# Optimization experiments

Measured on AMD Instinct MI355X. Metric: run time of the kernel, lower is better.

The kernel has to match this reference:

```python
import jax, jax.numpy as jnp
import numpy as np

MARGIN = 0.2
EPS = 1e-6  # torch.pairwise_distance adds eps to the difference before the norm


def setup_inputs() -> dict:
    key = jax.random.key(0)
    k1, k2, k3 = jax.random.split(key, 3)
    B, D = 8192, 128
    emb1 = jax.random.normal(k1, (B, D), dtype=jnp.float32)
    emb2 = jax.random.normal(k2, (B, D), dtype=jnp.float32)
    target = jax.random.randint(k3, (B,), 0, 2, dtype=jnp.int64)
    return {"emb1": emb1, "emb2": emb2, "target": target}


def reference(emb1, emb2, target):
    B, D = emb1.shape
    # torch.pairwise_distance(a, b) = ||a - b + EPS||_2; expand the square:
    # |a-b+eps|^2 = |a|^2 + |b|^2 - 2 a.b + 2*eps*(sum(a)-sum(b)) + D*eps^2
    sq = (
        jnp.sum(emb1 * emb1, axis=-1)[:, None]
        + jnp.sum(emb2 * emb2, axis=-1)[None, :]
        - 2.0 * (emb1 @ emb2.T)
        + 2.0 * EPS * (jnp.sum(emb1, axis=-1)[:, None] - jnp.sum(emb2, axis=-1)[None, :])
        + D * EPS * EPS
    )
    dist = jnp.sqrt(jnp.maximum(sq, 0.0))  # [B, B]: dist[i, j] = ||emb1[i] - emb2[j] + eps||

    pos = target == 1
    neg = target == 0
    # hardest positive: max over columns j with target[j]==1; hardest negative: min over target[j]==0
    pos_max = jnp.max(jnp.where(pos[None, :], dist, -jnp.inf), axis=1)  # [B]
    neg_min = jnp.min(jnp.where(neg[None, :], dist, jnp.inf), axis=1)   # [B]
    per_anchor = jnp.maximum(pos_max - neg_min + MARGIN, 0.0)
    anchor_w = pos.astype(dist.dtype)
    # mean over anchors (rows i with target[i]==1)
    return jnp.sum(per_anchor * anchor_w) / jnp.sum(anchor_w)
```

## Files before the change

kernel.cpp:

```cpp
#include <hip/hip_runtime.h>
#include <hip/hip_bf16.h>
#include <math.h>


#define DDIM   128
#define SPLITS 8
#define MARGIN 0.2f
#define EPS    1e-6f
#define SENT   1e30f

typedef unsigned short ushort_t;
typedef __attribute__((ext_vector_type(8))) short short8;
typedef __attribute__((ext_vector_type(8))) unsigned short ushort8;
typedef __attribute__((ext_vector_type(4))) float f32x4;

__device__ __forceinline__ ushort_t f2bf(float f) {
    unsigned int u = __float_as_uint(f);
    u = (u + 0x7FFFu + ((u >> 16) & 1u)) >> 16;
    return (ushort_t)u;
}

__global__ void prep_kernel(const float* __restrict__ e1, const float* __restrict__ e2,
                            const int* __restrict__ target,
                            float* __restrict__ rowterm,
                            float* __restrict__ cpos, float* __restrict__ cneg, int B) {
    int w    = (blockIdx.x * blockDim.x + threadIdx.x) >> 6;
    int lane = threadIdx.x & 63;
    if (w >= 2 * B) return;
    bool first = (w < B);
    int r = first ? w : w - B;
    const float* src = (first ? e1 : e2) + (size_t)r * DDIM;
    float2 v = *(const float2*)(src + lane * 2);
    float s = v.x + v.y;
    float n = v.x * v.x + v.y * v.y;
    #pragma unroll
    for (int off = 32; off > 0; off >>= 1) {
        s += __shfl_down(s, off, 64);
        n += __shfl_down(n, off, 64);
    }
    if (lane == 0) {
        if (first) {
            rowterm[r] = n + 2.f * EPS * s + (float)DDIM * EPS * EPS;
        } else {
            float ct = n - 2.f * EPS * s;
            int tg = target[r];
            cpos[r] = (tg == 1) ? ct : -SENT;
            cneg[r] = (tg == 0) ? ct :  SENT;
        }
    }
}

__device__ __forceinline__ void stage_tile(const float* __restrict__ g,
                                           ushort_t* __restrict__ lds, int tid) {
    #pragma unroll
    for (int it = 0; it < 8; ++it) {
        int idx = it * 256 + tid;
        int r   = idx >> 4;
        int c8  = idx & 15;
        const float* src = g + (size_t)r * DDIM + c8 * 8;
        float4 v0 = *(const float4*)src;
        float4 v1 = *(const float4*)(src + 4);
        ushort8 o;
        o[0] = f2bf(v0.x); o[1] = f2bf(v0.y); o[2] = f2bf(v0.z); o[3] = f2bf(v0.w);
        o[4] = f2bf(v1.x); o[5] = f2bf(v1.y); o[6] = f2bf(v1.z); o[7] = f2bf(v1.w);
        int pos = c8 ^ (r & 15);
        *(ushort8*)(lds + r * DDIM + pos * 8) = o;
    }
}

__global__ __launch_bounds__(256, 2)
void tile_kernel(const float* __restrict__ e1, const float* __restrict__ e2,
                 const float* __restrict__ cpos, const float* __restrict__ cneg,
                 float* __restrict__ pmp, float* __restrict__ nmp, int B) {
    __shared__ __align__(16) ushort_t As[128 * DDIM];
    __shared__ __align__(16) ushort_t Bs[128 * DDIM];

    const int tid = threadIdx.x;
    const int w   = tid >> 6;
    const int l   = tid & 63;
    const int lq  = l >> 4;
    const int lm  = l & 15;
    const int row0 = blockIdx.x * 128;
    const int colSpan = B / SPLITS;
    const int col0 = blockIdx.y * colSpan;
    const int nTiles = colSpan / 128;

    stage_tile(e1 + (size_t)row0 * DDIM, As, tid);

    const int wr = (w >> 1) * 64;
    const int wc = (w & 1) * 64;

    float pm[4][4], nm[4][4];
    #pragma unroll
    for (int i = 0; i < 4; ++i)
        #pragma unroll
        for (int r = 0; r < 4; ++r) { pm[i][r] = -SENT; nm[i][r] = SENT; }

    const ushort_t* aRow = As + (wr + lm) * DDIM;
    const ushort_t* bRow = Bs + (wc + lm) * DDIM;

    for (int t = 0; t < nTiles; ++t) {
        if (t) __syncthreads();
        stage_tile(e2 + (size_t)(col0 + t * 128) * DDIM, Bs, tid);
        __syncthreads();

        f32x4 acc[4][4];
        #pragma unroll
        for (int i = 0; i < 4; ++i)
            #pragma unroll
            for (int j = 0; j < 4; ++j)
                acc[i][j] = (f32x4){0.f, 0.f, 0.f, 0.f};

        #pragma unroll
        for (int kk = 0; kk < DDIM; kk += 32) {
            const int co = (((lq + (kk >> 3)) ^ lm) << 3);
            short8 af[4], bf[4];
            #pragma unroll
            for (int i = 0; i < 4; ++i)
                af[i] = *(const short8*)(aRow + i * 16 * DDIM + co);
            #pragma unroll
            for (int j = 0; j < 4; ++j)
                bf[j] = *(const short8*)(bRow + j * 16 * DDIM + co);
            #pragma unroll
            for (int i = 0; i < 4; ++i)
                #pragma unroll
                for (int j = 0; j < 4; ++j)
                    acc[i][j] = __builtin_amdgcn_mfma_f32_16x16x32_bf16(
                                    af[i], bf[j], acc[i][j], 0, 0, 0);
        }

        #pragma unroll
        for (int j = 0; j < 4; ++j) {
            int col = col0 + t * 128 + wc + j * 16 + lm;
            float cp = cpos[col];
            float cn = cneg[col];
            #pragma unroll
            for (int i = 0; i < 4; ++i)
                #pragma unroll
                for (int r = 0; r < 4; ++r) {
                    float d = acc[i][j][r];
                    pm[i][r] = fmaxf(pm[i][r], fmaf(-2.f, d, cp));
                    nm[i][r] = fminf(nm[i][r], fmaf(-2.f, d, cn));
                }
        }
    }

    #pragma unroll
    for (int m = 1; m < 16; m <<= 1) {
        #pragma unroll
        for (int i = 0; i < 4; ++i)
            #pragma unroll
            for (int r = 0; r < 4; ++r) {
                pm[i][r] = fmaxf(pm[i][r], __shfl_xor(pm[i][r], m, 64));
                nm[i][r] = fminf(nm[i][r], __shfl_xor(nm[i][r], m, 64));
            }
    }

    __syncthreads();
    float* smP = (float*)As;
    float* smN = smP + 128;
    if ((w & 1) == 1 && lm == 0) {
        #pragma unroll
        for (int i = 0; i < 4; ++i)
            #pragma unroll
            for (int r = 0; r < 4; ++r) {
                int lr = wr + i * 16 + lq * 4 + r;
                smP[lr] = pm[i][r];
                smN[lr] = nm[i][r];
            }
    }
    __syncthreads();
    if ((w & 1) == 0 && lm == 0) {
        #pragma unroll
        for (int i = 0; i < 4; ++i)
            #pragma unroll
            for (int r = 0; r < 4; ++r) {
                int lr  = wr + i * 16 + lq * 4 + r;
                int row = row0 + lr;
                pmp[(size_t)blockIdx.y * B + row] = fmaxf(pm[i][r], smP[lr]);
                nmp[(size_t)blockIdx.y * B + row] = fminf(nm[i][r], smN[lr]);
            }
    }
}

__global__ void reduce_kernel(const float* __restrict__ pmp, const float* __restrict__ nmp,
                              const float* __restrict__ rowterm, const int* __restrict__ target,
                              float* __restrict__ out, int B) {
    float s = 0.f, c = 0.f;
    for (int row = threadIdx.x; row < B; row += blockDim.x) {
        float pmv = -SENT, nmv = SENT;
        #pragma unroll
        for (int sp = 0; sp < SPLITS; ++sp) {
            pmv = fmaxf(pmv, pmp[(size_t)sp * B + row]);
            nmv = fminf(nmv, nmp[(size_t)sp * B + row]);
        }
        float rt = rowterm[row];
        float dp = sqrtf(fmaxf(rt + pmv, 0.f));
        float dn = sqrtf(fmaxf(rt + nmv, 0.f));
        if (target[row] == 1) {
            s += fmaxf(dp - dn + MARGIN, 0.f);
            c += 1.f;
        }
    }
    #pragma unroll
    for (int off = 32; off > 0; off >>= 1) {
        s += __shfl_down(s, off, 64);
        c += __shfl_down(c, off, 64);
    }
    __shared__ float ls[16], lc[16];
    int wv = threadIdx.x >> 6, ln = threadIdx.x & 63;
    if (ln == 0) { ls[wv] = s; lc[wv] = c; }
    __syncthreads();
    if (threadIdx.x == 0) {
        float ss = 0.f, cc = 0.f;
        int nw = blockDim.x >> 6;
        for (int i = 0; i < nw; ++i) { ss += ls[i]; cc += lc[i]; }
        out[0] = ss / cc;
    }
}

extern "C" void kernel_launch(void* const* d_in, const int* in_sizes, int n_in,
                              void* d_out, int out_size, void* d_ws, size_t ws_size,
                              hipStream_t stream) {
    const float* e1     = (const float*)d_in[0];
    const float* e2     = (const float*)d_in[1];
    const int*   target = (const int*)d_in[2];
    float* out = (float*)d_out;
    const int B = in_sizes[2];

    float* p = (float*)d_ws;
    float* rowterm = p;              p += B;
    float* cpos    = p;              p += B;
    float* cneg    = p;              p += B;
    float* pmp     = p;              p += (size_t)SPLITS * B;
    float* nmp     = p;

    {
        int blocks = (2 * B + 3) / 4;
        prep_kernel<<<blocks, 256, 0, stream>>>(e1, e2, target, rowterm, cpos, cneg, B);
    }
    {
        dim3 grid(B / 128, SPLITS);
        tile_kernel<<<grid, 256, 0, stream>>>(e1, e2, cpos, cneg, pmp, nmp, B);
    }
    reduce_kernel<<<1, 1024, 0, stream>>>(pmp, nmp, rowterm, target, out, B);
}
```

Before: 99.32 us.

## Pre-convert embeddings to bf16 and stage tiles via direct global-to-LDS loads

The prep kernel now writes bf16 copies of both embedding matrices, so the tile kernel no longer reloads fp32 data and converts it on every column tile. The tile kernel then stages tiles with global_load_lds DMA into a padded chunk layout, which removes the VGPR round trip and drops the XOR swizzle. The final reduction is spread over 32 blocks that combine through atomics and a ticket counter instead of running as a single block. This adds an extra bf16 write pass and workspace in prep, and relies on the padded pitch to avoid LDS bank conflicts.

```diff
diff --git a/kernel.cpp b/kernel.cpp
--- a/kernel.cpp
+++ b/kernel.cpp
@@ -9,9 +9,12 @@
 #define EPS    1e-6f
 #define SENT   1e30f
 
+#define CHUNK_PITCH 1056
+#define WAVE_SPAN   (8 * CHUNK_PITCH)
+#define TILE_BYTES  (4 * WAVE_SPAN)
+
 typedef unsigned short ushort_t;
 typedef __attribute__((ext_vector_type(8))) short short8;
-typedef __attribute__((ext_vector_type(8))) unsigned short ushort8;
 typedef __attribute__((ext_vector_type(4))) float f32x4;
 
 __device__ __forceinline__ ushort_t f2bf(float f) {
@@ -20,10 +23,22 @@
     return (ushort_t)u;
 }
 
+__device__ __forceinline__ void g2lds16(const ushort_t* g, void* lds) {
+    __builtin_amdgcn_global_load_lds(
+        (const __attribute__((address_space(1))) unsigned int*)g,
+        (__attribute__((address_space(3))) unsigned int*)lds,
+        16, 0, 0);
+}
+
 __global__ void prep_kernel(const float* __restrict__ e1, const float* __restrict__ e2,
                             const int* __restrict__ target,
+                            ushort_t* __restrict__ e1b, ushort_t* __restrict__ e2b,
                             float* __restrict__ rowterm,
-                            float* __restrict__ cpos, float* __restrict__ cneg, int B) {
+                            float* __restrict__ cpos, float* __restrict__ cneg,
+                            float* __restrict__ redsum, int* __restrict__ ticket, int B) {
+    if (blockIdx.x == 0 && threadIdx.x == 0) {
+        redsum[0] = 0.f; redsum[1] = 0.f; *ticket = 0;
+    }
     int w    = (blockIdx.x * blockDim.x + threadIdx.x) >> 6;
     int lane = threadIdx.x & 63;
     if (w >= 2 * B) return;
@@ -31,6 +46,9 @@
     int r = first ? w : w - B;
     const float* src = (first ? e1 : e2) + (size_t)r * DDIM;
     float2 v = *(const float2*)(src + lane * 2);
+    ushort_t* dst = (first ? e1b : e2b) + (size_t)r * DDIM;
+    ushort2 o; o.x = f2bf(v.x); o.y = f2bf(v.y);
+    *(ushort2*)(dst + lane * 2) = o;
     float s = v.x + v.y;
     float n = v.x * v.x + v.y * v.y;
     #pragma unroll
@@ -50,30 +68,22 @@
     }
 }
 
-__device__ __forceinline__ void stage_tile(const float* __restrict__ g,
-                                           ushort_t* __restrict__ lds, int tid) {
-    #pragma unroll
-    for (int it = 0; it < 8; ++it) {
-        int idx = it * 256 + tid;
-        int r   = idx >> 4;
-        int c8  = idx & 15;
-        const float* src = g + (size_t)r * DDIM + c8 * 8;
-        float4 v0 = *(const float4*)src;
-        float4 v1 = *(const float4*)(src + 4);
-        ushort8 o;
-        o[0] = f2bf(v0.x); o[1] = f2bf(v0.y); o[2] = f2bf(v0.z); o[3] = f2bf(v0.w);
-        o[4] = f2bf(v1.x); o[5] = f2bf(v1.y); o[6] = f2bf(v1.z); o[7] = f2bf(v1.w);
-        int pos = c8 ^ (r & 15);
-        *(ushort8*)(lds + r * DDIM + pos * 8) = o;
-    }
+__device__ __forceinline__ void stage_tile_dma(const ushort_t* __restrict__ gRow0,
+                                               unsigned char* __restrict__ lds,
+                                               int w, int l) {
+    const ushort_t* g = gRow0 + (size_t)(w * 32) * DDIM + l * 8;
+    unsigned char* lp = lds + w * WAVE_SPAN;
+    #pragma unroll
+    for (int it = 0; it < 8; ++it)
+        g2lds16(g + it * 512, lp + it * CHUNK_PITCH);
 }
 
 __global__ __launch_bounds__(256, 2)
-void tile_kernel(const float* __restrict__ e1, const float* __restrict__ e2,
+void tile_kernel(const ushort_t* __restrict__ e1b, const ushort_t* __restrict__ e2b,
                  const float* __restrict__ cpos, const float* __restrict__ cneg,
                  float* __restrict__ pmp, float* __restrict__ nmp, int B) {
-    __shared__ __align__(16) ushort_t As[128 * DDIM];
-    __shared__ __align__(16) ushort_t Bs[128 * DDIM];
+    __shared__ __align__(16) unsigned char As[TILE_BYTES];
+    __shared__ __align__(16) unsigned char Bs[TILE_BYTES];
 
     const int tid = threadIdx.x;
     const int w   = tid >> 6;
@@ -85,7 +95,7 @@
     const int col0 = blockIdx.y * colSpan;
     const int nTiles = colSpan / 128;
 
-    stage_tile(e1 + (size_t)row0 * DDIM, As, tid);
+    stage_tile_dma(e1b + (size_t)row0 * DDIM, As, w, l);
 
     const int wr = (w >> 1) * 64;
     const int wc = (w & 1) * 64;
@@ -96,12 +106,14 @@
         #pragma unroll
         for (int r = 0; r < 4; ++r) { pm[i][r] = -SENT; nm[i][r] = SENT; }
 
-    const ushort_t* aRow = As + (wr + lm) * DDIM;
-    const ushort_t* bRow = Bs + (wc + lm) * DDIM;
+    const unsigned char* aLane = As + ((wr >> 2) + (lm >> 2)) * CHUNK_PITCH
+                                    + (lm & 3) * 256 + lq * 16;
+    const unsigned char* bLane = Bs + ((wc >> 2) + (lm >> 2)) * CHUNK_PITCH
+                                    + (lm & 3) * 256 + lq * 16;
 
     for (int t = 0; t < nTiles; ++t) {
         if (t) __syncthreads();
-        stage_tile(e2 + (size_t)(col0 + t * 128) * DDIM, Bs, tid);
+        stage_tile_dma(e2b + (size_t)(col0 + t * 128) * DDIM, Bs, w, l);
         __syncthreads();
 
         f32x4 acc[4][4];
@@ -113,14 +125,14 @@
 
         #pragma unroll
         for (int kk = 0; kk < DDIM; kk += 32) {
-            const int co = (((lq + (kk >> 3)) ^ lm) << 3);
+            const int ko = kk * 2;
             short8 af[4], bf[4];
             #pragma unroll
             for (int i = 0; i < 4; ++i)
-                af[i] = *(const short8*)(aRow + i * 16 * DDIM + co);
+                af[i] = *(const short8*)(aLane + i * (4 * CHUNK_PITCH) + ko);
             #pragma unroll
             for (int j = 0; j < 4; ++j)
-                bf[j] = *(const short8*)(bRow + j * 16 * DDIM + co);
+                bf[j] = *(const short8*)(bLane + j * (4 * CHUNK_PITCH) + ko);
             #pragma unroll
             for (int i = 0; i < 4; ++i)
                 #pragma unroll
@@ -185,9 +197,11 @@
 
 __global__ void reduce_kernel(const float* __restrict__ pmp, const float* __restrict__ nmp,
                               const float* __restrict__ rowterm, const int* __restrict__ target,
+                              float* __restrict__ redsum, int* __restrict__ ticket,
                               float* __restrict__ out, int B) {
+    int row = blockIdx.x * blockDim.x + threadIdx.x;
     float s = 0.f, c = 0.f;
-    for (int row = threadIdx.x; row < B; row += blockDim.x) {
+    {
         float pmv = -SENT, nmv = SENT;
         #pragma unroll
         for (int sp = 0; sp < SPLITS; ++sp) {
@@ -198,8 +212,8 @@
         float dp = sqrtf(fmaxf(rt + pmv, 0.f));
         float dn = sqrtf(fmaxf(rt + nmv, 0.f));
         if (target[row] == 1) {
-            s += fmaxf(dp - dn + MARGIN, 0.f);
-            c += 1.f;
+            s = fmaxf(dp - dn + MARGIN, 0.f);
+            c = 1.f;
         }
     }
     #pragma unroll
@@ -207,15 +221,23 @@
         s += __shfl_down(s, off, 64);
         c += __shfl_down(c, off, 64);
     }
-    __shared__ float ls[16], lc[16];
+    __shared__ float ls[4], lc[4];
     int wv = threadIdx.x >> 6, ln = threadIdx.x & 63;
     if (ln == 0) { ls[wv] = s; lc[wv] = c; }
     __syncthreads();
     if (threadIdx.x == 0) {
-        float ss = 0.f, cc = 0.f;
-        int nw = blockDim.x >> 6;
-        for (int i = 0; i < nw; ++i) { ss += ls[i]; cc += lc[i]; }
-        out[0] = ss / cc;
+        float ss = ls[0] + ls[1] + ls[2] + ls[3];
+        float cc = lc[0] + lc[1] + lc[2] + lc[3];
+        atomicAdd(&redsum[0], ss);
+        atomicAdd(&redsum[1], cc);
+        __threadfence();
+        int done = atomicAdd(ticket, 1);
+        if (done == (int)gridDim.x - 1) {
+            __threadfence();
+            float fs = __hip_atomic_load(&redsum[0], __ATOMIC_RELAXED, __HIP_MEMORY_SCOPE_AGENT);
+            float fc = __hip_atomic_load(&redsum[1], __ATOMIC_RELAXED, __HIP_MEMORY_SCOPE_AGENT);
+            out[0] = fs / fc;
+        }
     }
 }
 
@@ -228,20 +250,26 @@
     float* out = (float*)d_out;
     const int B = in_sizes[2];
 
-    float* p = (float*)d_ws;
-    float* rowterm = p;              p += B;
-    float* cpos    = p;              p += B;
-    float* cneg    = p;              p += B;
-    float* pmp     = p;              p += (size_t)SPLITS * B;
-    float* nmp     = p;
+    char* p = (char*)d_ws;
+    ushort_t* e1b  = (ushort_t*)p;   p += (size_t)B * DDIM * 2;
+    ushort_t* e2b  = (ushort_t*)p;   p += (size_t)B * DDIM * 2;
+    float* rowterm = (float*)p;      p += (size_t)B * 4;
+    float* cpos    = (float*)p;      p += (size_t)B * 4;
+    float* cneg    = (float*)p;      p += (size_t)B * 4;
+    float* pmp     = (float*)p;      p += (size_t)SPLITS * B * 4;
+    float* nmp     = (float*)p;      p += (size_t)SPLITS * B * 4;
+    float* redsum  = (float*)p;      p += 2 * 4;
+    int*   ticket  = (int*)p;
 
     {
         int blocks = (2 * B + 3) / 4;
-        prep_kernel<<<blocks, 256, 0, stream>>>(e1, e2, target, rowterm, cpos, cneg, B);
+        prep_kernel<<<blocks, 256, 0, stream>>>(e1, e2, target, e1b, e2b,
+                                                rowterm, cpos, cneg, redsum, ticket, B);
     }
     {
         dim3 grid(B / 128, SPLITS);
-        tile_kernel<<<grid, 256, 0, stream>>>(e1, e2, cpos, cneg, pmp, nmp, B);
-    }
-    reduce_kernel<<<1, 1024, 0, stream>>>(pmp, nmp, rowterm, target, out, B);
-}
+        tile_kernel<<<grid, 256, 0, stream>>>(e1b, e2b, cpos, cneg, pmp, nmp, B);
+    }
+    reduce_kernel<<<32, 256, 0, stream>>>(pmp, nmp, rowterm, target,
+                                          redsum, ticket, out, B);
+}
```

Measured after the change: 94.04 us. -5.3%, faster.

## Fuse prep and reduce into tile kernel with atomics and last-block finish

Applied to the files above, without the earlier changes.

Drops the separate prep kernel by computing row and column norm/sum statistics while staging tiles into LDS. Per-row partial max/min results now go through order-preserving unsigned atomics, and the last block to finish, chosen with a ticket counter, does the final reduction, so the reduce kernel is gone. The A-operand fragments are also kept in registers across all column tiles instead of being reloaded from LDS each time. The cost is redundant column-stat work on every block, extra shuffles during staging, more register pressure, global atomic traffic, and a small init kernel.

```diff
diff --git a/kernel.cpp b/kernel.cpp
--- a/kernel.cpp
+++ b/kernel.cpp
@@ -20,60 +20,32 @@
     return (ushort_t)u;
 }
 
-__global__ void prep_kernel(const float* __restrict__ e1, const float* __restrict__ e2,
-                            const int* __restrict__ target,
-                            float* __restrict__ rowterm,
-                            float* __restrict__ cpos, float* __restrict__ cneg, int B) {
-    int w    = (blockIdx.x * blockDim.x + threadIdx.x) >> 6;
-    int lane = threadIdx.x & 63;
-    if (w >= 2 * B) return;
-    bool first = (w < B);
-    int r = first ? w : w - B;
-    const float* src = (first ? e1 : e2) + (size_t)r * DDIM;
-    float2 v = *(const float2*)(src + lane * 2);
-    float s = v.x + v.y;
-    float n = v.x * v.x + v.y * v.y;
-    #pragma unroll
-    for (int off = 32; off > 0; off >>= 1) {
-        s += __shfl_down(s, off, 64);
-        n += __shfl_down(n, off, 64);
-    }
-    if (lane == 0) {
-        if (first) {
-            rowterm[r] = n + 2.f * EPS * s + (float)DDIM * EPS * EPS;
-        } else {
-            float ct = n - 2.f * EPS * s;
-            int tg = target[r];
-            cpos[r] = (tg == 1) ? ct : -SENT;
-            cneg[r] = (tg == 0) ? ct :  SENT;
-        }
-    }
-}
-
-__device__ __forceinline__ void stage_tile(const float* __restrict__ g,
-                                           ushort_t* __restrict__ lds, int tid) {
-    #pragma unroll
-    for (int it = 0; it < 8; ++it) {
-        int idx = it * 256 + tid;
-        int r   = idx >> 4;
-        int c8  = idx & 15;
-        const float* src = g + (size_t)r * DDIM + c8 * 8;
-        float4 v0 = *(const float4*)src;
-        float4 v1 = *(const float4*)(src + 4);
-        ushort8 o;
-        o[0] = f2bf(v0.x); o[1] = f2bf(v0.y); o[2] = f2bf(v0.z); o[3] = f2bf(v0.w);
-        o[4] = f2bf(v1.x); o[5] = f2bf(v1.y); o[6] = f2bf(v1.z); o[7] = f2bf(v1.w);
-        int pos = c8 ^ (r & 15);
-        *(ushort8*)(lds + r * DDIM + pos * 8) = o;
-    }
+__device__ __forceinline__ unsigned enc(float f) {
+    unsigned b = __float_as_uint(f);
+    return (b & 0x80000000u) ? ~b : (b | 0x80000000u);
+}
+__device__ __forceinline__ float dec(unsigned k) {
+    unsigned b = (k & 0x80000000u) ? (k & 0x7FFFFFFFu) : ~k;
+    return __uint_as_float(b);
+}
+
+__global__ void init_kernel(unsigned* __restrict__ pmkey, unsigned* __restrict__ nmkey,
+                            int* __restrict__ ticket, int B) {
+    int i = blockIdx.x * blockDim.x + threadIdx.x;
+    if (i < B) { pmkey[i] = 0u; nmkey[i] = 0u; }
+    if (i == 0) *ticket = 0;
 }
 
 __global__ __launch_bounds__(256, 2)
 void tile_kernel(const float* __restrict__ e1, const float* __restrict__ e2,
-                 const float* __restrict__ cpos, const float* __restrict__ cneg,
-                 float* __restrict__ pmp, float* __restrict__ nmp, int B) {
+                 const int* __restrict__ target,
+                 float* __restrict__ rowterm,
+                 unsigned* __restrict__ pmkey, unsigned* __restrict__ nmkey,
+                 int* __restrict__ ticket, float* __restrict__ out, int B) {
     __shared__ __align__(16) ushort_t As[128 * DDIM];
     __shared__ __align__(16) ushort_t Bs[128 * DDIM];
+    __shared__ float ctP[128], ctN[128];
+    __shared__ int lastSh;
 
     const int tid = threadIdx.x;
     const int w   = tid >> 6;
@@ -84,11 +56,87 @@
     const int colSpan = B / SPLITS;
     const int col0 = blockIdx.y * colSpan;
     const int nTiles = colSpan / 128;
-
-    stage_tile(e1 + (size_t)row0 * DDIM, As, tid);
+    const int nBlocks = gridDim.x * gridDim.y;
+
+    {
+        const float* g = e1 + (size_t)row0 * DDIM;
+        const bool doStats = (blockIdx.y == 0);
+        #pragma unroll
+        for (int it = 0; it < 8; ++it) {
+            int idx = it * 256 + tid;
+            int r   = idx >> 4;
+            int c8  = idx & 15;
+            const float* src = g + (size_t)r * DDIM + c8 * 8;
+            float4 v0 = *(const float4*)src;
+            float4 v1 = *(const float4*)(src + 4);
+            ushort8 o;
+            o[0]=f2bf(v0.x); o[1]=f2bf(v0.y); o[2]=f2bf(v0.z); o[3]=f2bf(v0.w);
+            o[4]=f2bf(v1.x); o[5]=f2bf(v1.y); o[6]=f2bf(v1.z); o[7]=f2bf(v1.w);
+            *(ushort8*)(As + r * DDIM + ((c8 ^ (r & 15)) << 3)) = o;
+            if (doStats) {
+                float s8 = (v0.x+v0.y)+(v0.z+v0.w)+(v1.x+v1.y)+(v1.z+v1.w);
+                float q8 = v0.x*v0.x+v0.y*v0.y+v0.z*v0.z+v0.w*v0.w
+                         + v1.x*v1.x+v1.y*v1.y+v1.z*v1.z+v1.w*v1.w;
+                #pragma unroll
+                for (int m = 1; m < 16; m <<= 1) {
+                    s8 += __shfl_xor(s8, m, 64);
+                    q8 += __shfl_xor(q8, m, 64);
+                }
+                if (lm == 0) {
+                    float rt = q8 + 2.f * EPS * s8 + (float)DDIM * EPS * EPS;
+                    atomicExch(&rowterm[row0 + r], rt);
+                }
+            }
+        }
+    }
 
     const int wr = (w >> 1) * 64;
     const int wc = (w & 1) * 64;
+
+    auto stageB = [&](int t) {
+        const float* g = e2 + (size_t)(col0 + t * 128) * DDIM;
+        const int* tg0 = target + col0 + t * 128;
+        #pragma unroll
+        for (int it = 0; it < 8; ++it) {
+            int idx = it * 256 + tid;
+            int r   = idx >> 4;
+            int c8  = idx & 15;
+            const float* src = g + (size_t)r * DDIM + c8 * 8;
+            float4 v0 = *(const float4*)src;
+            float4 v1 = *(const float4*)(src + 4);
+            ushort8 o;
+            o[0]=f2bf(v0.x); o[1]=f2bf(v0.y); o[2]=f2bf(v0.z); o[3]=f2bf(v0.w);
+            o[4]=f2bf(v1.x); o[5]=f2bf(v1.y); o[6]=f2bf(v1.z); o[7]=f2bf(v1.w);
+            *(ushort8*)(Bs + r * DDIM + ((c8 ^ (r & 15)) << 3)) = o;
+            float s8 = (v0.x+v0.y)+(v0.z+v0.w)+(v1.x+v1.y)+(v1.z+v1.w);
+            float q8 = v0.x*v0.x+v0.y*v0.y+v0.z*v0.z+v0.w*v0.w
+                     + v1.x*v1.x+v1.y*v1.y+v1.z*v1.z+v1.w*v1.w;
+            #pragma unroll
+            for (int m = 1; m < 16; m <<= 1) {
+                s8 += __shfl_xor(s8, m, 64);
+                q8 += __shfl_xor(q8, m, 64);
+            }
+            if (lm == 0) {
+                float ct = q8 - 2.f * EPS * s8;
+                int tg = tg0[r];
+                ctP[r] = (tg == 1) ? ct : -SENT;
+                ctN[r] = (tg == 0) ? ct :  SENT;
+            }
+        }
+    };
+
+    stageB(0);
+    __syncthreads();
+
+    const ushort_t* aRow = As + (wr + lm) * DDIM;
+    const ushort_t* bRow = Bs + (wc + lm) * DDIM;
+    short8 afr[4][4];
+    #pragma unroll
+    for (int i = 0; i < 4; ++i)
+        #pragma unroll
+        for (int k4 = 0; k4 < 4; ++k4)
+            afr[i][k4] = *(const short8*)(aRow + i * 16 * DDIM
+                                          + (((lq + k4 * 4) ^ lm) << 3));
 
     float pm[4][4], nm[4][4];
     #pragma unroll
@@ -96,14 +144,7 @@
         #pragma unroll
         for (int r = 0; r < 4; ++r) { pm[i][r] = -SENT; nm[i][r] = SENT; }
 
-    const ushort_t* aRow = As + (wr + lm) * DDIM;
-    const ushort_t* bRow = Bs + (wc + lm) * DDIM;
-
     for (int t = 0; t < nTiles; ++t) {
-        if (t) __syncthreads();
-        stage_tile(e2 + (size_t)(col0 + t * 128) * DDIM, Bs, tid);
-        __syncthreads();
-
         f32x4 acc[4][4];
         #pragma unroll
         for (int i = 0; i < 4; ++i)
@@ -113,11 +154,9 @@
 
         #pragma unroll
         for (int kk = 0; kk < DDIM; kk += 32) {
+            const int k4 = kk >> 5;
             const int co = (((lq + (kk >> 3)) ^ lm) << 3);
-            short8 af[4], bf[4];
-            #pragma unroll
-            for (int i = 0; i < 4; ++i)
-                af[i] = *(const short8*)(aRow + i * 16 * DDIM + co);
+            short8 bf[4];
             #pragma unroll
             for (int j = 0; j < 4; ++j)
                 bf[j] = *(const short8*)(bRow + j * 16 * DDIM + co);
@@ -126,14 +165,14 @@
                 #pragma unroll
                 for (int j = 0; j < 4; ++j)
                     acc[i][j] = __builtin_amdgcn_mfma_f32_16x16x32_bf16(
-                                    af[i], bf[j], acc[i][j], 0, 0, 0);
+                                    afr[i][k4], bf[j], acc[i][j], 0, 0, 0);
         }
 
         #pragma unroll
         for (int j = 0; j < 4; ++j) {
-            int col = col0 + t * 128 + wc + j * 16 + lm;
-            float cp = cpos[col];
-            float cn = cneg[col];
+            int lc = wc + j * 16 + lm;
+            float cp = ctP[lc];
+            float cn = ctN[lc];
             #pragma unroll
             for (int i = 0; i < 4; ++i)
                 #pragma unroll
@@ -143,6 +182,12 @@
                     nm[i][r] = fminf(nm[i][r], fmaf(-2.f, d, cn));
                 }
         }
+
+        if (t + 1 < nTiles) {
+            __syncthreads();
+            stageB(t + 1);
+            __syncthreads();
+        }
     }
 
     #pragma unroll
@@ -177,45 +222,49 @@
             for (int r = 0; r < 4; ++r) {
                 int lr  = wr + i * 16 + lq * 4 + r;
                 int row = row0 + lr;
-                pmp[(size_t)blockIdx.y * B + row] = fmaxf(pm[i][r], smP[lr]);
-                nmp[(size_t)blockIdx.y * B + row] = fminf(nm[i][r], smN[lr]);
-            }
-    }
-}
-
-__global__ void reduce_kernel(const float* __restrict__ pmp, const float* __restrict__ nmp,
-                              const float* __restrict__ rowterm, const int* __restrict__ target,
-                              float* __restrict__ out, int B) {
-    float s = 0.f, c = 0.f;
-    for (int row = threadIdx.x; row < B; row += blockDim.x) {
-        float pmv = -SENT, nmv = SENT;
-        #pragma unroll
-        for (int sp = 0; sp < SPLITS; ++sp) {
-            pmv = fmaxf(pmv, pmp[(size_t)sp * B + row]);
-            nmv = fminf(nmv, nmp[(size_t)sp * B + row]);
-        }
-        float rt = rowterm[row];
-        float dp = sqrtf(fmaxf(rt + pmv, 0.f));
-        float dn = sqrtf(fmaxf(rt + nmv, 0.f));
-        if (target[row] == 1) {
-            s += fmaxf(dp - dn + MARGIN, 0.f);
-            c += 1.f;
-        }
-    }
-    #pragma unroll
-    for (int off = 32; off > 0; off >>= 1) {
-        s += __shfl_down(s, off, 64);
-        c += __shfl_down(c, off, 64);
-    }
-    __shared__ float ls[16], lc[16];
-    int wv = threadIdx.x >> 6, ln = threadIdx.x & 63;
-    if (ln == 0) { ls[wv] = s; lc[wv] = c; }
-    __syncthreads();
-    if (threadIdx.x == 0) {
-        float ss = 0.f, cc = 0.f;
-        int nw = blockDim.x >> 6;
-        for (int i = 0; i < nw; ++i) { ss += ls[i]; cc += lc[i]; }
-        out[0] = ss / cc;
+                float p = fmaxf(pm[i][r], smP[lr]);
+                float n = fminf(nm[i][r], smN[lr]);
+                atomicMax(&pmkey[row], enc(p));
+                atomicMax(&nmkey[row], enc(-n));
+            }
+    }
+
+    __threadfence();
+    __syncthreads();
+    if (tid == 0) {
+        int done = atomicAdd(ticket, 1);
+        lastSh = (done == nBlocks - 1);
+    }
+    __syncthreads();
+    if (lastSh) {
+        __threadfence();
+        float s = 0.f, c = 0.f;
+        for (int row = tid; row < B; row += 256) {
+            unsigned kp = __hip_atomic_load(&pmkey[row], __ATOMIC_RELAXED,
+                                            __HIP_MEMORY_SCOPE_AGENT);
+            unsigned kn = __hip_atomic_load(&nmkey[row], __ATOMIC_RELAXED,
+                                            __HIP_MEMORY_SCOPE_AGENT);
+            float rt = __hip_atomic_load(&rowterm[row], __ATOMIC_RELAXED,
+                                         __HIP_MEMORY_SCOPE_AGENT);
+            float pmv = dec(kp);
+            float nmv = -dec(kn);
+            float dp = sqrtf(fmaxf(rt + pmv, 0.f));
+            float dn = sqrtf(fmaxf(rt + nmv, 0.f));
+            if (target[row] == 1) {
+                s += fmaxf(dp - dn + MARGIN, 0.f);
+                c += 1.f;
+            }
+        }
+        #pragma unroll
+        for (int off = 32; off > 0; off >>= 1) {
+            s += __shfl_down(s, off, 64);
+            c += __shfl_down(c, off, 64);
+        }
+        if (l == 0) { ctP[w] = s; ctN[w] = c; }
+        __syncthreads();
+        if (tid == 0)
+            out[0] = (ctP[0] + ctP[1] + ctP[2] + ctP[3])
+                   / (ctN[0] + ctN[1] + ctN[2] + ctN[3]);
     }
 }
 
@@ -228,20 +277,15 @@
     float* out = (float*)d_out;
     const int B = in_sizes[2];
 
-    float* p = (float*)d_ws;
-    float* rowterm = p;              p += B;
-    float* cpos    = p;              p += B;
-    float* cneg    = p;              p += B;
-    float* pmp     = p;              p += (size_t)SPLITS * B;
-    float* nmp     = p;
-
-    {
-        int blocks = (2 * B + 3) / 4;
-        prep_kernel<<<blocks, 256, 0, stream>>>(e1, e2, target, rowterm, cpos, cneg, B);
-    }
-    {
-        dim3 grid(B / 128, SPLITS);
-        tile_kernel<<<grid, 256, 0, stream>>>(e1, e2, cpos, cneg, pmp, nmp, B);
-    }
-    reduce_kernel<<<1, 1024, 0, stream>>>(pmp, nmp, rowterm, target, out, B);
-}
+    char* p = (char*)d_ws;
+    float*    rowterm = (float*)p;    p += (size_t)B * 4;
+    unsigned* pmkey   = (unsigned*)p; p += (size_t)B * 4;
+    unsigned* nmkey   = (unsigned*)p; p += (size_t)B * 4;
+    int*      ticket  = (int*)p;
+
+    init_kernel<<<(B + 255) / 256, 256, 0, stream>>>(pmkey, nmkey, ticket, B);
+
+    dim3 grid(B / 128, SPLITS);
+    tile_kernel<<<grid, 256, 0, stream>>>(e1, e2, target, rowterm,
+                                          pmkey, nmkey, ticket, out, B);
+}
```

Result: slower. 167.4 us (+68.6%).
